# Kernel tuning notes

Hardware: AMD Instinct MI355X
Metric: run time of the kernel (lower is better)

Reference implementation:

```python
import jax, jax.numpy as jnp
import numpy as np
from math import factorial, sqrt

# ---- e3nn-style real Wigner-3j (Clebsch-Gordan) construction ----
L1, L2, LOUT, LMID = 3, 3, 3, 4

def _cg_coef(j1, m1, j2, m2, j3, m3):
    if m1 + m2 != m3:
        return 0.0
    f = factorial
    vmin = max(0, j2 - j3 - m1, j1 - j3 + m2)
    vmax = min(j1 + j2 - j3, j1 - m1, j2 + m2)
    pref = sqrt((2 * j3 + 1) * f(j3 + j1 - j2) * f(j3 - j1 + j2) * f(j1 + j2 - j3) / f(j1 + j2 + j3 + 1))
    pref *= sqrt(f(j3 + m3) * f(j3 - m3) * f(j1 + m1) * f(j1 - m1) * f(j2 + m2) * f(j2 - m2))
    s = 0.0
    for v in range(vmin, vmax + 1):
        s += (-1) ** v / (f(v) * f(j1 + j2 - j3 - v) * f(j1 - m1 - v) * f(j2 + m2 - v)
                          * f(j3 - j2 + m1 + v) * f(j3 - j1 - m2 + v))
    return pref * s

def _su2_cg(l1, l2, l3):
    C = np.zeros((2 * l1 + 1, 2 * l2 + 1, 2 * l3 + 1))
    for m1 in range(-l1, l1 + 1):
        for m2 in range(-l2, l2 + 1):
            m3 = m1 + m2
            if -l3 <= m3 <= l3:
                C[l1 + m1, l2 + m2, l3 + m3] = _cg_coef(l1, m1, l2, m2, l3, m3)
    return C

def _q(l):  # real->complex SH change of basis (e3nn convention)
    q = np.zeros((2 * l + 1, 2 * l + 1), dtype=np.complex128)
    for m in range(-l, 0):
        q[l + m, l + abs(m)] = 1 / np.sqrt(2)
        q[l + m, l - abs(m)] = -1j / np.sqrt(2)
    q[l, l] = 1.0
    for m in range(1, l + 1):
        q[l + m, l + abs(m)] = (-1) ** m / np.sqrt(2)
        q[l + m, l - abs(m)] = 1j * (-1) ** m / np.sqrt(2)
    return (-1j) ** l * q

def _w3j(l1, l2, l3):
    C = _su2_cg(l1, l2, l3).astype(np.complex128)
    C = np.einsum('ij,kl,mn,ikn->jlm', _q(l1), _q(l2), np.conj(_q(l3).T), C)
    C = np.real(C)
    return (C / np.linalg.norm(C)).astype(np.float32)

def _instructions(lmax1, lmax2, lmax_out):
    ins = [(a, b, c)
           for a in range(lmax1 + 1) for b in range(lmax2 + 1) for c in range(lmax_out + 1)
           if abs(a - b) <= c <= a + b and (a + b + c) % 2 == 0]
    cnt = {}
    for _, _, c in ins:
        cnt[c] = cnt.get(c, 0) + 1
    # normalization='component', path_normalization='element' with all mul=1
    pw = np.array([sqrt((2 * c + 1) / cnt[c]) for _, _, c in ins], dtype=np.float32)
    return ins, pw

INS1, PW1 = _instructions(L1, L2, LMID)      # 27 paths
INS21, PW21 = _instructions(L1, LMID, LOUT)  # 27 paths
INS22, PW22 = _instructions(L2, LMID, LOUT)  # 27 paths
W3J = {k: jnp.asarray(_w3j(*k)) for k in set(INS1) | set(INS21) | set(INS22)}

def _tp(x, y, w, ins, pw, lmax_out):
    # FullyConnectedTensorProduct with multiplicity-1 SH irreps.
    # x: [E, (l1+1)^2], y: [E, (l2+1)^2] -> [E, (lmax_out+1)^2]
    out = jnp.zeros((x.shape[0], (lmax_out + 1) ** 2), dtype=x.dtype)
    for i, (a, b, c) in enumerate(ins):
        xa = x[:, a * a:(a + 1) ** 2]
        yb = y[:, b * b:(b + 1) ** 2]
        z = jnp.einsum('ijk,ei,ej->ek', W3J[(a, b, c)], xa, yb)
        out = out.at[:, c * c:(c + 1) ** 2].add((pw[i] * w[i]) * z)
    return out

E, C = 200000, 16
B = (LOUT + 1) ** 2  # 16

def setup_inputs() -> dict:
    k = jax.random.split(jax.random.key(0), 5)
    return {
        'x': jax.random.normal(k[0], (E, B, C), jnp.float32),
        'y': jax.random.normal(k[1], (E, B, C), jnp.float32),
        'w1': jax.random.normal(k[2], (len(INS1),), jnp.float32),
        'w21': jax.random.normal(k[3], (len(INS21),), jnp.float32),
        'w22': jax.random.normal(k[4], (len(INS22),), jnp.float32),
    }

def reference(x, y, w1, w21, w22):
    xm = x.mean(2)  # [E, 16]
    ym = y.mean(2)  # [E, 16]
    mid = _tp(xm, ym, w1, INS1, PW1, LMID)  # [E, 25]
    out = (x + y
           + _tp(xm, mid, w21, INS21, PW21, LOUT)[..., None]
           + _tp(ym, mid, w22, INS22, PW22, LOUT)[..., None])
    return out
```

## Files before the change

kernel.cpp:

```cpp
#include <hip/hip_runtime.h>


struct W3JT { double v[9][9][9]; };

constexpr double dfact(int n) { double r = 1.0; for (int i = 2; i <= n; ++i) r *= (double)i; return r; }

constexpr double csqrt(double x) {
  if (x <= 0.0) return 0.0;
  double g = x > 1.0 ? x : 1.0;
  for (int i = 0; i < 80; ++i) g = 0.5 * (g + x / g);
  return g;
}

constexpr double cg_coef(int j1, int m1, int j2, int m2, int j3, int m3) {
  if (m1 + m2 != m3) return 0.0;
  int vmin = 0;
  if (j2 - j3 - m1 > vmin) vmin = j2 - j3 - m1;
  if (j1 - j3 + m2 > vmin) vmin = j1 - j3 + m2;
  int vmax = j1 + j2 - j3;
  if (j1 - m1 < vmax) vmax = j1 - m1;
  if (j2 + m2 < vmax) vmax = j2 + m2;
  double pref = csqrt((2.0 * j3 + 1.0) * dfact(j3 + j1 - j2) * dfact(j3 - j1 + j2) * dfact(j1 + j2 - j3) / dfact(j1 + j2 + j3 + 1));
  pref *= csqrt(dfact(j3 + m3) * dfact(j3 - m3) * dfact(j1 + m1) * dfact(j1 - m1) * dfact(j2 + m2) * dfact(j2 - m2));
  double s = 0.0;
  for (int v = vmin; v <= vmax; ++v) {
    double t = 1.0 / (dfact(v) * dfact(j1 + j2 - j3 - v) * dfact(j1 - m1 - v) * dfact(j2 + m2 - v) * dfact(j3 - j2 + m1 + v) * dfact(j3 - j1 - m2 + v));
    s += (v & 1) ? -t : t;
  }
  return pref * s;
}

struct QCol { int n; int row[2]; double re[2]; double im[2]; };

constexpr QCol qcol(int l, int col) {
  QCol q{};
  const int lm = l & 3;
  const double pr = (lm == 0) ? 1.0 : (lm == 2) ? -1.0 : 0.0;
  const double pi = (lm == 1) ? -1.0 : (lm == 3) ? 1.0 : 0.0;
  const int mu = col - l;
  const int am = mu < 0 ? -mu : mu;
  const double is2 = 0.70710678118654752440;
  if (mu == 0) {
    q.n = 1; q.row[0] = l;
    q.re[0] = pr; q.im[0] = pi;
  } else {
    const double s = (am & 1) ? -1.0 : 1.0;
    double a0, b0, a1, b1;
    if (mu > 0) { a0 = is2; b0 = 0.0;  a1 = s * is2; b1 = 0.0; }
    else        { a0 = 0.0; b0 = -is2; a1 = 0.0;     b1 = s * is2; }
    q.n = 2;
    q.row[0] = l - am; q.row[1] = l + am;
    q.re[0] = a0 * pr - b0 * pi; q.im[0] = a0 * pi + b0 * pr;
    q.re[1] = a1 * pr - b1 * pi; q.im[1] = a1 * pi + b1 * pr;
  }
  return q;
}

constexpr W3JT make_w3j(int l1, int l2, int l3) {
  W3JT R{};
  double C[9][9][9]{};
  for (int m1 = -l1; m1 <= l1; ++m1)
    for (int m2 = -l2; m2 <= l2; ++m2) {
      int m3 = m1 + m2;
      if (m3 >= -l3 && m3 <= l3)
        C[l1 + m1][l2 + m2][l3 + m3] = cg_coef(l1, m1, l2, m2, l3, m3);
    }
  double nrm = 0.0;
  for (int j = 0; j < 2 * l1 + 1; ++j) {
    QCol q1 = qcol(l1, j);
    for (int l = 0; l < 2 * l2 + 1; ++l) {
      QCol q2 = qcol(l2, l);
      for (int m = 0; m < 2 * l3 + 1; ++m) {
        QCol q3 = qcol(l3, m);
        double re = 0.0;
        for (int a = 0; a < q1.n; ++a)
          for (int b = 0; b < q2.n; ++b)
            for (int c = 0; c < q3.n; ++c) {
              double cv = C[q1.row[a]][q2.row[b]][q3.row[c]];
              if (cv == 0.0) continue;
              double ar = q1.re[a], ai = q1.im[a];
              double br = q2.re[b], bi = q2.im[b];
              double cr = q3.re[c], ci = -q3.im[c];
              double abr = ar * br - ai * bi;
              double abi = ar * bi + ai * br;
              double prr = abr * cr - abi * ci;
              re += prr * cv;
            }
        R.v[j][l][m] = re;
        nrm += re * re;
      }
    }
  }
  double n = csqrt(nrm);
  if (n > 0.0)
    for (int j = 0; j < 2 * l1 + 1; ++j)
      for (int l = 0; l < 2 * l2 + 1; ++l)
        for (int m = 0; m < 2 * l3 + 1; ++m)
          R.v[j][l][m] /= n;
  return R;
}

constexpr int CNT1[5] = {4, 6, 7, 6, 4};
constexpr int CNT2[4] = {4, 7, 8, 8};

#define NZCHK(V) ((V) > 1e-12 || (V) < -1e-12)

#define TP_MID(IDX, A, B, C) do { \
  constexpr W3JT T = make_w3j(A, B, C); \
  constexpr double PW = csqrt((2.0 * (C) + 1.0) / (double)CNT1[(C)]); \
  const float wi = w1p[IDX]; \
  float u[2 * (A) + 1]; \
  _Pragma("unroll") for (int i = 0; i < 2 * (A) + 1; ++i) u[i] = wi * xm[(A) * (A) + i]; \
  _Pragma("unroll") for (int i = 0; i < 2 * (A) + 1; ++i) { \
    _Pragma("unroll") for (int j = 0; j < 2 * (B) + 1; ++j) { \
      const float p_ = u[i] * ym[(B) * (B) + j]; \
      _Pragma("unroll") for (int k = 0; k < 2 * (C) + 1; ++k) { \
        if (NZCHK(T.v[i][j][k])) \
          mid[(C) * (C) + k] = __builtin_fmaf((float)(T.v[i][j][k] * PW), p_, mid[(C) * (C) + k]); \
      } \
    } \
  } \
} while (0)

#define TP_OUT(IDX, A, B, C) do { \
  constexpr W3JT T = make_w3j(A, B, C); \
  constexpr double PW = csqrt((2.0 * (C) + 1.0) / (double)CNT2[(C)]); \
  const float wa = w21p[IDX]; \
  const float wb = w22p[IDX]; \
  float u[2 * (A) + 1]; \
  _Pragma("unroll") for (int i = 0; i < 2 * (A) + 1; ++i) \
    u[i] = wa * xm[(A) * (A) + i] + wb * ym[(A) * (A) + i]; \
  _Pragma("unroll") for (int i = 0; i < 2 * (A) + 1; ++i) { \
    _Pragma("unroll") for (int j = 0; j < 2 * (B) + 1; ++j) { \
      const float p_ = u[i] * mid[(B) * (B) + j]; \
      _Pragma("unroll") for (int k = 0; k < 2 * (C) + 1; ++k) { \
        if (NZCHK(T.v[i][j][k])) \
          tv[(C) * (C) + k] = __builtin_fmaf((float)(T.v[i][j][k] * PW), p_, tv[(C) * (C) + k]); \
      } \
    } \
  } \
} while (0)

__global__ __launch_bounds__(256) void cg2_fused(
    const float4* __restrict__ x4, const float4* __restrict__ y4,
    const float* __restrict__ w1p, const float* __restrict__ w21p,
    const float* __restrict__ w22p, float4* __restrict__ o4, int E)
{
  const int t = blockIdx.x * 256 + threadIdx.x;
  const int e = t >> 2;
  if (e >= E) return;
  const int g = t & 3;
  const int base = e * 64 + g;

  float4 s[16];
  float xm[16], ym[16];
#pragma unroll
  for (int k = 0; k < 16; ++k) {
    const float4 xv = x4[base + 4 * k];
    const float4 yv = y4[base + 4 * k];
    s[k].x = xv.x + yv.x; s[k].y = xv.y + yv.y;
    s[k].z = xv.z + yv.z; s[k].w = xv.w + yv.w;
    float rx = (xv.x + xv.y) + (xv.z + xv.w);
    float ry = (yv.x + yv.y) + (yv.z + yv.w);
    rx += __shfl_xor(rx, 1); rx += __shfl_xor(rx, 2);
    ry += __shfl_xor(ry, 1); ry += __shfl_xor(ry, 2);
    xm[k] = rx * (1.0f / 16.0f);
    ym[k] = ry * (1.0f / 16.0f);
  }

  float mid[25];
#pragma unroll
  for (int k = 0; k < 25; ++k) mid[k] = 0.f;

  TP_MID( 0, 0, 0, 0);
  TP_MID( 1, 0, 1, 1);
  TP_MID( 2, 0, 2, 2);
  TP_MID( 3, 0, 3, 3);
  TP_MID( 4, 1, 0, 1);
  TP_MID( 5, 1, 1, 0);
  TP_MID( 6, 1, 1, 2);
  TP_MID( 7, 1, 2, 1);
  TP_MID( 8, 1, 2, 3);
  TP_MID( 9, 1, 3, 2);
  TP_MID(10, 1, 3, 4);
  TP_MID(11, 2, 0, 2);
  TP_MID(12, 2, 1, 1);
  TP_MID(13, 2, 1, 3);
  TP_MID(14, 2, 2, 0);
  TP_MID(15, 2, 2, 2);
  TP_MID(16, 2, 2, 4);
  TP_MID(17, 2, 3, 1);
  TP_MID(18, 2, 3, 3);
  TP_MID(19, 3, 0, 3);
  TP_MID(20, 3, 1, 2);
  TP_MID(21, 3, 1, 4);
  TP_MID(22, 3, 2, 1);
  TP_MID(23, 3, 2, 3);
  TP_MID(24, 3, 3, 0);
  TP_MID(25, 3, 3, 2);
  TP_MID(26, 3, 3, 4);

  float tv[16];
#pragma unroll
  for (int k = 0; k < 16; ++k) tv[k] = 0.f;

  TP_OUT( 0, 0, 0, 0);
  TP_OUT( 1, 0, 1, 1);
  TP_OUT( 2, 0, 2, 2);
  TP_OUT( 3, 0, 3, 3);
  TP_OUT( 4, 1, 0, 1);
  TP_OUT( 5, 1, 1, 0);
  TP_OUT( 6, 1, 1, 2);
  TP_OUT( 7, 1, 2, 1);
  TP_OUT( 8, 1, 2, 3);
  TP_OUT( 9, 1, 3, 2);
  TP_OUT(10, 1, 4, 3);
  TP_OUT(11, 2, 0, 2);
  TP_OUT(12, 2, 1, 1);
  TP_OUT(13, 2, 1, 3);
  TP_OUT(14, 2, 2, 0);
  TP_OUT(15, 2, 2, 2);
  TP_OUT(16, 2, 3, 1);
  TP_OUT(17, 2, 3, 3);
  TP_OUT(18, 2, 4, 2);
  TP_OUT(19, 3, 0, 3);
  TP_OUT(20, 3, 1, 2);
  TP_OUT(21, 3, 2, 1);
  TP_OUT(22, 3, 2, 3);
  TP_OUT(23, 3, 3, 0);
  TP_OUT(24, 3, 3, 2);
  TP_OUT(25, 3, 4, 1);
  TP_OUT(26, 3, 4, 3);

#pragma unroll
  for (int k = 0; k < 16; ++k) {
    float4 o;
    o.x = s[k].x + tv[k];
    o.y = s[k].y + tv[k];
    o.z = s[k].z + tv[k];
    o.w = s[k].w + tv[k];
    o4[base + 4 * k] = o;
  }
}

extern "C" void kernel_launch(void* const* d_in, const int* in_sizes, int n_in,
                              void* d_out, int out_size, void* d_ws, size_t ws_size,
                              hipStream_t stream) {
  const float4* x4 = (const float4*)d_in[0];
  const float4* y4 = (const float4*)d_in[1];
  const float* w1p = (const float*)d_in[2];
  const float* w21p = (const float*)d_in[3];
  const float* w22p = (const float*)d_in[4];
  float4* o4 = (float4*)d_out;

  const int E = in_sizes[0] / 256;
  const int total = E * 4;
  const int block = 256;
  const int grid = (total + block - 1) / block;

  cg2_fused<<<grid, block, 0, stream>>>(x4, y4, w1p, w21p, w22p, o4, E);
}
```

Baseline: 129.9 us.

## Map one edge per thread and reload inputs instead of holding sums

Switches from four threads per edge (with shuffle reductions for the channel means) to one thread per edge, so the tensor-product work is no longer computed redundantly by four lanes. The kernel drops the held x+y registers and re-reads x and y from global memory for the final output write, aiming to cut register pressure. In exchange each thread reads 256 contiguous bytes per row, so loads across a wavefront are strided by 256 floats and poorly coalesced. The second read of x and y also relies on cache hits.

Result: slower. 387.0 us (+197.8%).

```diff
diff --git a/kernel.cpp b/kernel.cpp
--- a/kernel.cpp
+++ b/kernel.cpp
@@ -141,31 +141,28 @@
   } \
 } while (0)
 
-__global__ __launch_bounds__(256) void cg2_fused(
+__global__ __launch_bounds__(256) void cg2_v2(
     const float4* __restrict__ x4, const float4* __restrict__ y4,
     const float* __restrict__ w1p, const float* __restrict__ w21p,
     const float* __restrict__ w22p, float4* __restrict__ o4, int E)
 {
-  const int t = blockIdx.x * 256 + threadIdx.x;
-  const int e = t >> 2;
+  const int e = blockIdx.x * 256 + threadIdx.x;
   if (e >= E) return;
-  const int g = t & 3;
-  const int base = e * 64 + g;
-
-  float4 s[16];
+  const int base = e * 64;
+
   float xm[16], ym[16];
 #pragma unroll
-  for (int k = 0; k < 16; ++k) {
-    const float4 xv = x4[base + 4 * k];
-    const float4 yv = y4[base + 4 * k];
-    s[k].x = xv.x + yv.x; s[k].y = xv.y + yv.y;
-    s[k].z = xv.z + yv.z; s[k].w = xv.w + yv.w;
-    float rx = (xv.x + xv.y) + (xv.z + xv.w);
-    float ry = (yv.x + yv.y) + (yv.z + yv.w);
-    rx += __shfl_xor(rx, 1); rx += __shfl_xor(rx, 2);
-    ry += __shfl_xor(ry, 1); ry += __shfl_xor(ry, 2);
-    xm[k] = rx * (1.0f / 16.0f);
-    ym[k] = ry * (1.0f / 16.0f);
+  for (int r = 0; r < 16; ++r) {
+    float sx = 0.f, sy = 0.f;
+#pragma unroll
+    for (int i = 0; i < 4; ++i) {
+      const float4 a = x4[base + 4 * r + i];
+      const float4 b = y4[base + 4 * r + i];
+      sx += (a.x + a.y) + (a.z + a.w);
+      sy += (b.x + b.y) + (b.z + b.w);
+    }
+    xm[r] = sx * (1.0f / 16.0f);
+    ym[r] = sy * (1.0f / 16.0f);
   }
 
   float mid[25];
@@ -233,13 +230,19 @@
   TP_OUT(26, 3, 4, 3);
 
 #pragma unroll
-  for (int k = 0; k < 16; ++k) {
-    float4 o;
-    o.x = s[k].x + tv[k];
-    o.y = s[k].y + tv[k];
-    o.z = s[k].z + tv[k];
-    o.w = s[k].w + tv[k];
-    o4[base + 4 * k] = o;
+  for (int r = 0; r < 16; ++r) {
+    const float t = tv[r];
+#pragma unroll
+    for (int i = 0; i < 4; ++i) {
+      const float4 a = x4[base + 4 * r + i];
+      const float4 b = y4[base + 4 * r + i];
+      float4 o;
+      o.x = a.x + b.x + t;
+      o.y = a.y + b.y + t;
+      o.z = a.z + b.z + t;
+      o.w = a.w + b.w + t;
+      o4[base + 4 * r + i] = o;
+    }
   }
 }
 
@@ -254,9 +257,8 @@
   float4* o4 = (float4*)d_out;
 
   const int E = in_sizes[0] / 256;
-  const int total = E * 4;
   const int block = 256;
-  const int grid = (total + block - 1) / block;
-
-  cg2_fused<<<grid, block, 0, stream>>>(x4, y4, w1p, w21p, w22p, o4, E);
-}
+  const int grid = (E + block - 1) / block;
+
+  cg2_v2<<<grid, block, 0, stream>>>(x4, y4, w1p, w21p, w22p, o4, E);
+}
```
